# Performance work log

Hardware: AMD Instinct MI355X
Metric: run time of the kernel (lower is better)

Reference implementation:

```python
import jax, jax.numpy as jnp
import numpy as np

EPS = 1e-12

def _l2norm(x):
    # F.normalize(p=2, dim=1)
    n = jnp.sqrt(jnp.sum(x * x, axis=1, keepdims=True))
    return x / jnp.maximum(n, EPS)

def _sage(h, c, W, b):
    # Bundler: Linear(concat(h, mean_neigh)) -> l2 normalize -> relu
    z = jnp.concatenate([h, c], axis=1) @ W + b
    return jax.nn.relu(_l2norm(z))

def _block_diag(blocks):
    # blocks: [B, K, K] -> dense [B*K, B*K] block-diagonal (torch.block_diag of per-graph S^T A S)
    B, K, _ = blocks.shape
    out = jnp.zeros((B * K, B * K), blocks.dtype)
    base = (jnp.arange(B) * K)[:, None, None]
    r = base + jnp.arange(K)[None, :, None]
    c = base + jnp.arange(K)[None, None, :]
    return out.at[r, c].set(blocks)

def setup_inputs() -> dict:
    key = jax.random.key(0)
    k0, k1, k2, k3, k4 = jax.random.split(key, 5)
    B, n, F, K, E = 64, 1024, 128, 128, 16384
    N = B * n
    h = jax.random.normal(k0, (N, F), dtype=jnp.float32)
    src_local = jax.random.randint(k1, (B, E), 0, n, dtype=jnp.int32)
    dst_local = jax.random.randint(k2, (B, E), 0, n, dtype=jnp.int32)
    s = 1.0 / np.sqrt(2 * F)
    W_feat = jax.random.normal(k3, (2 * F, F), dtype=jnp.float32) * s
    b_feat = jnp.zeros((F,), dtype=jnp.float32)
    W_pool = jax.random.normal(k4, (2 * F, K), dtype=jnp.float32) * s
    b_pool = jnp.zeros((K,), dtype=jnp.float32)
    return {"h": h, "src_local": src_local, "dst_local": dst_local,
            "W_feat": W_feat, "b_feat": b_feat, "W_pool": W_pool, "b_pool": b_pool}

def reference(h, src_local, dst_local, W_feat, b_feat, W_pool, b_pool):
    N, F = h.shape
    B, E = src_local.shape
    n = N // B
    K = W_pool.shape[1]
    # per-graph local edge ids -> global ids (batched graph)
    off = (jnp.arange(B, dtype=src_local.dtype) * n)[:, None]
    src = (src_local + off).reshape(-1)  # [B*E]
    dst = (dst_local + off).reshape(-1)
    # MeanAggregator: c[i] = mean over in-neighbors (edges src->dst) of h[src]
    deg = jax.ops.segment_sum(jnp.ones((B * E,), h.dtype), dst, num_segments=N)
    c = jax.ops.segment_sum(h[src], dst, num_segments=N) / jnp.maximum(deg, 1.0)[:, None]
    feat = _sage(h, c, W_feat, b_feat)                     # [N, F]
    assign = jax.nn.softmax(_sage(h, c, W_pool, b_pool), axis=1)  # [N, K] per-graph soft assignment
    # adj_external(transpose=True): adj[u, v] = 1 for edge (u -> v)
    # AS[u] = sum over edges (u->v) of assign[v]
    AS = jax.ops.segment_sum(assign[dst], src, num_segments=N)    # [N, K]
    S_r = assign.reshape(B, n, K)
    AS_r = AS.reshape(B, n, K)
    feat_r = feat.reshape(B, n, F)
    # h_new = S^T feat (block-diagonal S => per-graph contraction)
    h_new = jnp.einsum('bnk,bnf->bkf', S_r, feat_r).reshape(B * K, F)
    # adj_new = S^T (adj S), block diagonal across graphs
    blocks = jnp.einsum('bnk,bnl->bkl', S_r, AS_r)
    adj_new = _block_diag(blocks)
    return adj_new, h_new
```

## Files before the change

kernel.cpp:

```cpp
#include <hip/hip_runtime.h>
#include <hip/hip_bf16.h>
#include <cstddef>

#define B_    64
#define NPG   1024
#define F_    128
#define K_    128
#define E_    16384
#define N_    (B_*NPG)
#define BE_   (B_*E_)
#define ADJ_DIM 8192
#define ADJ_ELEMS 67108864UL

typedef __bf16 bf16x8 __attribute__((ext_vector_type(8)));
typedef float  f32x4  __attribute__((ext_vector_type(4)));
typedef unsigned short u16x8 __attribute__((ext_vector_type(8)));

__device__ inline unsigned short f2b(float f) {
  __bf16 b = (__bf16)f;
  return *reinterpret_cast<unsigned short*>(&b);
}
__device__ inline unsigned packbf(float x, float y) {
  return (unsigned)f2b(x) | ((unsigned)f2b(y) << 16);
}
__device__ inline void addrow(float* a, uint4 v) {
  a[0] += __uint_as_float(v.x << 16);
  a[1] += __uint_as_float(v.x & 0xffff0000u);
  a[2] += __uint_as_float(v.y << 16);
  a[3] += __uint_as_float(v.y & 0xffff0000u);
  a[4] += __uint_as_float(v.z << 16);
  a[5] += __uint_as_float(v.z & 0xffff0000u);
  a[6] += __uint_as_float(v.w << 16);
  a[7] += __uint_as_float(v.w & 0xffff0000u);
}

__global__ void k_hbf(const float* __restrict__ h, unsigned short* __restrict__ hb) {
  int i = blockIdx.x * 256 + threadIdx.x;
  float4 v = reinterpret_cast<const float4*>(h)[i];
  ushort4 o;
  o.x = f2b(v.x); o.y = f2b(v.y); o.z = f2b(v.z); o.w = f2b(v.w);
  reinterpret_cast<ushort4*>(hb)[i] = o;
}

__global__ void k_count(const int* __restrict__ srcl, const int* __restrict__ dstl,
                        int* __restrict__ deg_in, int* __restrict__ deg_out) {
  int i = blockIdx.x * 256 + threadIdx.x;
  int b = i >> 14;
  int base = b << 10;
  atomicAdd(&deg_in[dstl[i] + base], 1);
  atomicAdd(&deg_out[srcl[i] + base], 1);
}

__global__ __launch_bounds__(1024) void k_scan(const int* __restrict__ deg,
                                               int* __restrict__ off, int* __restrict__ cur) {
  int b = blockIdx.x, t = threadIdx.x;
  int v = deg[b * NPG + t];
  int lane = t & 63, wid = t >> 6;
  int x = v;
  #pragma unroll
  for (int d = 1; d < 64; d <<= 1) {
    int y = __shfl_up(x, d, 64);
    if (lane >= d) x += y;
  }
  __shared__ int wsum[16];
  if (lane == 63) wsum[wid] = x;
  __syncthreads();
  if (t < 16) {
    int s = wsum[t];
    #pragma unroll
    for (int d = 1; d < 16; d <<= 1) {
      int y = __shfl_up(s, d, 16);
      if (t >= d) s += y;
    }
    wsum[t] = s;
  }
  __syncthreads();
  int woff = wid ? wsum[wid - 1] : 0;
  int o = b * E_ + woff + x - v;
  off[b * NPG + t] = o;
  cur[b * NPG + t] = o;
}

__global__ void k_build(const int* __restrict__ srcl, const int* __restrict__ dstl,
                        int* __restrict__ cur_in, int* __restrict__ cur_out,
                        int* __restrict__ ebd_src, int* __restrict__ ebs_dst) {
  int i = blockIdx.x * 256 + threadIdx.x;
  int b = i >> 14;
  int base = b << 10;
  int s = srcl[i] + base, d = dstl[i] + base;
  int p = atomicAdd(&cur_in[d], 1);
  ebd_src[p] = s;
  int q = atomicAdd(&cur_out[s], 1);
  ebs_dst[q] = d;
}

template<int ROWSTRIDE, bool MEAN, bool ZERO>
__global__ void k_gather(const unsigned short* __restrict__ rows, const int* __restrict__ elist,
                         const int* __restrict__ off, const int* __restrict__ deg,
                         unsigned short* __restrict__ outb, float* __restrict__ adj) {
  if (ZERO) {
    float4 z4 = make_float4(0.f, 0.f, 0.f, 0.f);
    float4* dst = reinterpret_cast<float4*>(adj) + (size_t)blockIdx.x * 1024 + threadIdx.x;
    #pragma unroll
    for (int r = 0; r < 4; ++r) dst[r * 256] = z4;
  }
  int w = threadIdx.x >> 6, lane = threadIdx.x & 63;
  int g = lane >> 4, li = lane & 15;
  int node = blockIdx.x * 4 + w;
  int o = off[node], d = deg[node];
  float acc[8];
  #pragma unroll
  for (int i = 0; i < 8; ++i) acc[i] = 0.f;
  const unsigned short* rbase = rows + li * 8;
  int e = o, end = o + d;
  while (e < end) {
    int cnt = end - e; if (cnt > 64) cnt = 64;
    int sidx = (lane < cnt) ? elist[e + lane] : 0;
    for (int t = 0; t * 4 < cnt; ++t) {
      int j = t * 4 + g;
      int s = __shfl(sidx, j, 64);
      if (j < cnt) {
        uint4 v = *reinterpret_cast<const uint4*>(rbase + (size_t)s * ROWSTRIDE);
        addrow(acc, v);
      }
    }
    e += cnt;
  }
  #pragma unroll
  for (int i = 0; i < 8; ++i) {
    acc[i] += __shfl_xor(acc[i], 16, 64);
    acc[i] += __shfl_xor(acc[i], 32, 64);
  }
  if (g == 0) {
    float sc = MEAN ? (1.0f / fmaxf((float)d, 1.0f)) : 1.0f;
    uint4 ov;
    ov.x = packbf(acc[0] * sc, acc[1] * sc);
    ov.y = packbf(acc[2] * sc, acc[3] * sc);
    ov.z = packbf(acc[4] * sc, acc[5] * sc);
    ov.w = packbf(acc[6] * sc, acc[7] * sc);
    *reinterpret_cast<uint4*>(outb + (size_t)node * 128 + li * 8) = ov;
  }
}

__global__ void k_wt(const float* __restrict__ Wf, const float* __restrict__ Wp,
                     __bf16* __restrict__ Wt) {
  int j = blockIdx.x;
  int k = threadIdx.x;
  const float* W = (j < 128) ? Wf : Wp;
  int jj = j & 127;
  Wt[j * 256 + k] = (__bf16)W[k * 128 + jj];
}

__global__ __launch_bounds__(512) void k_gemm(const __bf16* __restrict__ hb,
                                              const __bf16* __restrict__ cb,
                                              const __bf16* __restrict__ Wt,
                                              const float* __restrict__ bfeat,
                                              const float* __restrict__ bpool,
                                              __bf16* __restrict__ Z) {
  __shared__ char smem[69632];
  __bf16* A_lds = (__bf16*)smem;
  __bf16* B_lds = (__bf16*)(smem + 8192);
  const int t = threadIdx.x;
  const int wid = t >> 6, lane = t & 63;
  const int wm = wid >> 1, wn = wid & 1;
  const int lo = lane & 15, hi = lane >> 4;
  const int m0 = blockIdx.x * 128;

  float bias[8];
  const float* bsrc = wn ? bpool : bfeat;
  #pragma unroll
  for (int nf = 0; nf < 8; ++nf) bias[nf] = bsrc[nf * 16 + lo];

  f32x4 acc[2][8];
  #pragma unroll
  for (int mf = 0; mf < 2; ++mf)
    #pragma unroll
    for (int nf = 0; nf < 8; ++nf) acc[mf][nf] = (f32x4){0.f, 0.f, 0.f, 0.f};

  const int am = t >> 2, akq = (t & 3) * 8;
  const int bj = t >> 1, bh = (t & 1) * 16;

  for (int ks = 0; ks < 8; ++ks) {
    const int kb = ks * 32;
    const __bf16* __restrict__ X = (kb < 128) ? hb : cb;
    const int kbb = kb & 127;
    *reinterpret_cast<bf16x8*>(A_lds + am * 32 + akq) =
        *reinterpret_cast<const bf16x8*>(X + (size_t)(m0 + am) * 128 + kbb + akq);
    {
      bf16x8 b0 = *reinterpret_cast<const bf16x8*>(Wt + bj * 256 + kb + bh);
      bf16x8 b1 = *reinterpret_cast<const bf16x8*>(Wt + bj * 256 + kb + bh + 8);
      *reinterpret_cast<bf16x8*>(B_lds + bj * 40 + bh) = b0;
      *reinterpret_cast<bf16x8*>(B_lds + bj * 40 + bh + 8) = b1;
    }
    __syncthreads();
    bf16x8 a[2], b[8];
    #pragma unroll
    for (int mf = 0; mf < 2; ++mf)
      a[mf] = *reinterpret_cast<const bf16x8*>(A_lds + (wm * 32 + mf * 16 + lo) * 32 + hi * 8);
    #pragma unroll
    for (int nf = 0; nf < 8; ++nf)
      b[nf] = *reinterpret_cast<const bf16x8*>(B_lds + (wn * 128 + nf * 16 + lo) * 40 + hi * 8);
    #pragma unroll
    for (int mf = 0; mf < 2; ++mf)
      #pragma unroll
      for (int nf = 0; nf < 8; ++nf)
        acc[mf][nf] = __builtin_amdgcn_mfma_f32_16x16x32_bf16(a[mf], b[nf], acc[mf][nf], 0, 0, 0);
    __syncthreads();
  }

  __bf16* obuf = (__bf16*)(smem + wid * 8704);
  #pragma unroll
  for (int mf = 0; mf < 2; ++mf) {
    #pragma unroll
    for (int r = 0; r < 4; ++r) {
      float v[8];
      #pragma unroll
      for (int nf = 0; nf < 8; ++nf) v[nf] = acc[mf][nf][r] + bias[nf];
      float ss = 0.f;
      #pragma unroll
      for (int nf = 0; nf < 8; ++nf) ss += v[nf] * v[nf];
      ss += __shfl_xor(ss, 1, 64); ss += __shfl_xor(ss, 2, 64);
      ss += __shfl_xor(ss, 4, 64); ss += __shfl_xor(ss, 8, 64);
      float rn = 1.0f / fmaxf(sqrtf(ss), 1e-12f);
      #pragma unroll
      for (int nf = 0; nf < 8; ++nf) v[nf] = fmaxf(v[nf] * rn, 0.f);
      if (wn) {
        float mx = v[0];
        #pragma unroll
        for (int nf = 1; nf < 8; ++nf) mx = fmaxf(mx, v[nf]);
        mx = fmaxf(mx, __shfl_xor(mx, 1, 64)); mx = fmaxf(mx, __shfl_xor(mx, 2, 64));
        mx = fmaxf(mx, __shfl_xor(mx, 4, 64)); mx = fmaxf(mx, __shfl_xor(mx, 8, 64));
        float es = 0.f;
        #pragma unroll
        for (int nf = 0; nf < 8; ++nf) { v[nf] = __expf(v[nf] - mx); es += v[nf]; }
        es += __shfl_xor(es, 1, 64); es += __shfl_xor(es, 2, 64);
        es += __shfl_xor(es, 4, 64); es += __shfl_xor(es, 8, 64);
        float inv = 1.0f / es;
        #pragma unroll
        for (int nf = 0; nf < 8; ++nf) v[nf] *= inv;
      }
      int row = mf * 16 + hi * 4 + r;
      #pragma unroll
      for (int nf = 0; nf < 8; ++nf) obuf[row * 136 + nf * 16 + lo] = (__bf16)v[nf];
    }
  }
  __syncthreads();
  #pragma unroll
  for (int i = 0; i < 8; ++i) {
    int r = i * 4 + hi;
    bf16x8 d = *reinterpret_cast<const bf16x8*>(obuf + r * 136 + lo * 8);
    int node = m0 + wm * 32 + r;
    *reinterpret_cast<bf16x8*>(Z + (size_t)node * 256 + wn * 128 + lo * 8) = d;
  }
}

__global__ __launch_bounds__(256) void k_poolm(const unsigned short* __restrict__ Zb,
                                               const unsigned short* __restrict__ ASb,
                                               float* __restrict__ h_new,
                                               float* __restrict__ adj) {
  const int blk = blockIdx.x;
  const int b = blk >> 2, ch = (blk >> 1) & 1, nh = blk & 1;
  const int n0 = b * NPG + nh * 512;
  __shared__ __align__(16) unsigned short ST[128 * 40];
  __shared__ __align__(16) unsigned short XT[128 * 40];
  const int t = threadIdx.x;
  const int wid = t >> 6, lane = t & 63;
  const int lo = lane & 15, hi = lane >> 4;
  const int wk = wid >> 1, wf = wid & 1;
  const int sn = t & 31, sc0 = (t >> 5) * 16;

  f32x4 acc[4][4];
  #pragma unroll
  for (int m = 0; m < 4; ++m)
    #pragma unroll
    for (int f = 0; f < 4; ++f) acc[m][f] = (f32x4){0.f, 0.f, 0.f, 0.f};

  for (int nc = 0; nc < 512; nc += 32) {
    int n = n0 + nc + sn;
    {
      u16x8 s0 = *reinterpret_cast<const u16x8*>(Zb + (size_t)n * 256 + 128 + sc0);
      u16x8 s1 = *reinterpret_cast<const u16x8*>(Zb + (size_t)n * 256 + 128 + sc0 + 8);
      #pragma unroll
      for (int i = 0; i < 8; ++i) ST[(sc0 + i) * 40 + sn] = s0[i];
      #pragma unroll
      for (int i = 0; i < 8; ++i) ST[(sc0 + 8 + i) * 40 + sn] = s1[i];
    }
    {
      const unsigned short* xr = ch ? (ASb + (size_t)n * 128 + sc0)
                                    : (Zb + (size_t)n * 256 + sc0);
      u16x8 x0 = *reinterpret_cast<const u16x8*>(xr);
      u16x8 x1 = *reinterpret_cast<const u16x8*>(xr + 8);
      #pragma unroll
      for (int i = 0; i < 8; ++i) XT[(sc0 + i) * 40 + sn] = x0[i];
      #pragma unroll
      for (int i = 0; i < 8; ++i) XT[(sc0 + 8 + i) * 40 + sn] = x1[i];
    }
    __syncthreads();
    bf16x8 a[4], bb[4];
    #pragma unroll
    for (int m = 0; m < 4; ++m)
      a[m] = *reinterpret_cast<const bf16x8*>(ST + (wk * 64 + m * 16 + lo) * 40 + hi * 8);
    #pragma unroll
    for (int f = 0; f < 4; ++f)
      bb[f] = *reinterpret_cast<const bf16x8*>(XT + (wf * 64 + f * 16 + lo) * 40 + hi * 8);
    #pragma unroll
    for (int m = 0; m < 4; ++m)
      #pragma unroll
      for (int f = 0; f < 4; ++f)
        acc[m][f] = __builtin_amdgcn_mfma_f32_16x16x32_bf16(a[m], bb[f], acc[m][f], 0, 0, 0);
    __syncthreads();
  }

  if (ch == 0) {
    #pragma unroll
    for (int m = 0; m < 4; ++m)
      #pragma unroll
      for (int f = 0; f < 4; ++f)
        #pragma unroll
        for (int r = 0; r < 4; ++r) {
          int k = wk * 64 + m * 16 + hi * 4 + r;
          int fc = wf * 64 + f * 16 + lo;
          atomicAdd(&h_new[(size_t)(b * 128 + k) * 128 + fc], acc[m][f][r]);
        }
  } else {
    #pragma unroll
    for (int m = 0; m < 4; ++m)
      #pragma unroll
      for (int f = 0; f < 4; ++f)
        #pragma unroll
        for (int r = 0; r < 4; ++r) {
          int k = wk * 64 + m * 16 + hi * 4 + r;
          int fc = wf * 64 + f * 16 + lo;
          atomicAdd(&adj[(size_t)(b * 128 + k) * ADJ_DIM + b * 128 + fc], acc[m][f][r]);
        }
  }
}

extern "C" void kernel_launch(void* const* d_in, const int* in_sizes, int n_in,
                              void* d_out, int out_size, void* d_ws, size_t ws_size,
                              hipStream_t stream) {
  (void)in_sizes; (void)n_in; (void)out_size; (void)ws_size;
  const float* h   = (const float*)d_in[0];
  const int* srcl  = (const int*)d_in[1];
  const int* dstl  = (const int*)d_in[2];
  const float* Wf  = (const float*)d_in[3];
  const float* bfe = (const float*)d_in[4];
  const float* Wp  = (const float*)d_in[5];
  const float* bpo = (const float*)d_in[6];

  float* out   = (float*)d_out;
  float* adj   = out;
  float* h_new = out + ADJ_ELEMS;

  char* W = (char*)d_ws;
  int* deg_in   = (int*)W;
  int* deg_out  = deg_in + N_;
  int* off_in   = deg_out + N_;
  int* cur_in   = off_in + N_;
  int* off_out  = cur_in + N_;
  int* cur_out  = off_out + N_;
  int* ebd_src  = cur_out + N_;
  int* ebs_dst  = ebd_src + BE_;
  unsigned short* hb  = (unsigned short*)(ebs_dst + BE_);
  unsigned short* cb  = hb + 8388608UL;
  unsigned short* Zb  = cb + 8388608UL;
  unsigned short* ASb = Zb + 16777216UL;
  __bf16* Wt          = (__bf16*)(ASb + 8388608UL);

  hipMemsetAsync(deg_in, 0, 2UL * N_ * sizeof(int), stream);
  hipMemsetAsync(h_new, 0, (size_t)B_ * K_ * F_ * sizeof(float), stream);
  k_hbf<<<8192, 256, 0, stream>>>(h, hb);
  k_wt<<<256, 256, 0, stream>>>(Wf, Wp, Wt);
  k_count<<<BE_ / 256, 256, 0, stream>>>(srcl, dstl, deg_in, deg_out);
  k_scan<<<B_, 1024, 0, stream>>>(deg_in, off_in, cur_in);
  k_scan<<<B_, 1024, 0, stream>>>(deg_out, off_out, cur_out);
  k_build<<<BE_ / 256, 256, 0, stream>>>(srcl, dstl, cur_in, cur_out, ebd_src, ebs_dst);
  k_gather<128, true, true><<<N_ / 4, 256, 0, stream>>>(hb, ebd_src, off_in, deg_in, cb, adj);
  k_gemm<<<N_ / 128, 512, 0, stream>>>((const __bf16*)hb, (const __bf16*)cb, Wt, bfe, bpo, (__bf16*)Zb);
  k_gather<256, false, false><<<N_ / 4, 256, 0, stream>>>(Zb + 128, ebs_dst, off_out, deg_out, ASb, nullptr);
  k_poolm<<<256, 256, 0, stream>>>(Zb, ASb, h_new, adj);
}
```

Before: 570.1 us.

## Replace CSR edge gathers with dense per-graph adjacency GEMMs on MFMA

Drops the CSR pipeline (degree counts, scans, bucket build, two sparse row gathers). Instead it scatters edge counts into a dense 1024x1024 fp32 adjacency block per graph and computes the neighbour mean and the A·S term as bf16 MFMA GEMMs. The h-to-bf16 conversion is folded into the feature GEMM's A-tile load, and zeroing of the adj output moves into that GEMM. This trades irregular gathers and atomics for a 256 MB dense matrix that must be zeroed and then read twice, so memory traffic goes up.

```diff
diff --git a/kernel.cpp b/kernel.cpp
--- a/kernel.cpp
+++ b/kernel.cpp
@@ -20,127 +20,6 @@
   __bf16 b = (__bf16)f;
   return *reinterpret_cast<unsigned short*>(&b);
 }
-__device__ inline unsigned packbf(float x, float y) {
-  return (unsigned)f2b(x) | ((unsigned)f2b(y) << 16);
-}
-__device__ inline void addrow(float* a, uint4 v) {
-  a[0] += __uint_as_float(v.x << 16);
-  a[1] += __uint_as_float(v.x & 0xffff0000u);
-  a[2] += __uint_as_float(v.y << 16);
-  a[3] += __uint_as_float(v.y & 0xffff0000u);
-  a[4] += __uint_as_float(v.z << 16);
-  a[5] += __uint_as_float(v.z & 0xffff0000u);
-  a[6] += __uint_as_float(v.w << 16);
-  a[7] += __uint_as_float(v.w & 0xffff0000u);
-}
-
-__global__ void k_hbf(const float* __restrict__ h, unsigned short* __restrict__ hb) {
-  int i = blockIdx.x * 256 + threadIdx.x;
-  float4 v = reinterpret_cast<const float4*>(h)[i];
-  ushort4 o;
-  o.x = f2b(v.x); o.y = f2b(v.y); o.z = f2b(v.z); o.w = f2b(v.w);
-  reinterpret_cast<ushort4*>(hb)[i] = o;
-}
-
-__global__ void k_count(const int* __restrict__ srcl, const int* __restrict__ dstl,
-                        int* __restrict__ deg_in, int* __restrict__ deg_out) {
-  int i = blockIdx.x * 256 + threadIdx.x;
-  int b = i >> 14;
-  int base = b << 10;
-  atomicAdd(&deg_in[dstl[i] + base], 1);
-  atomicAdd(&deg_out[srcl[i] + base], 1);
-}
-
-__global__ __launch_bounds__(1024) void k_scan(const int* __restrict__ deg,
-                                               int* __restrict__ off, int* __restrict__ cur) {
-  int b = blockIdx.x, t = threadIdx.x;
-  int v = deg[b * NPG + t];
-  int lane = t & 63, wid = t >> 6;
-  int x = v;
-  #pragma unroll
-  for (int d = 1; d < 64; d <<= 1) {
-    int y = __shfl_up(x, d, 64);
-    if (lane >= d) x += y;
-  }
-  __shared__ int wsum[16];
-  if (lane == 63) wsum[wid] = x;
-  __syncthreads();
-  if (t < 16) {
-    int s = wsum[t];
-    #pragma unroll
-    for (int d = 1; d < 16; d <<= 1) {
-      int y = __shfl_up(s, d, 16);
-      if (t >= d) s += y;
-    }
-    wsum[t] = s;
-  }
-  __syncthreads();
-  int woff = wid ? wsum[wid - 1] : 0;
-  int o = b * E_ + woff + x - v;
-  off[b * NPG + t] = o;
-  cur[b * NPG + t] = o;
-}
-
-__global__ void k_build(const int* __restrict__ srcl, const int* __restrict__ dstl,
-                        int* __restrict__ cur_in, int* __restrict__ cur_out,
-                        int* __restrict__ ebd_src, int* __restrict__ ebs_dst) {
-  int i = blockIdx.x * 256 + threadIdx.x;
-  int b = i >> 14;
-  int base = b << 10;
-  int s = srcl[i] + base, d = dstl[i] + base;
-  int p = atomicAdd(&cur_in[d], 1);
-  ebd_src[p] = s;
-  int q = atomicAdd(&cur_out[s], 1);
-  ebs_dst[q] = d;
-}
-
-template<int ROWSTRIDE, bool MEAN, bool ZERO>
-__global__ void k_gather(const unsigned short* __restrict__ rows, const int* __restrict__ elist,
-                         const int* __restrict__ off, const int* __restrict__ deg,
-                         unsigned short* __restrict__ outb, float* __restrict__ adj) {
-  if (ZERO) {
-    float4 z4 = make_float4(0.f, 0.f, 0.f, 0.f);
-    float4* dst = reinterpret_cast<float4*>(adj) + (size_t)blockIdx.x * 1024 + threadIdx.x;
-    #pragma unroll
-    for (int r = 0; r < 4; ++r) dst[r * 256] = z4;
-  }
-  int w = threadIdx.x >> 6, lane = threadIdx.x & 63;
-  int g = lane >> 4, li = lane & 15;
-  int node = blockIdx.x * 4 + w;
-  int o = off[node], d = deg[node];
-  float acc[8];
-  #pragma unroll
-  for (int i = 0; i < 8; ++i) acc[i] = 0.f;
-  const unsigned short* rbase = rows + li * 8;
-  int e = o, end = o + d;
-  while (e < end) {
-    int cnt = end - e; if (cnt > 64) cnt = 64;
-    int sidx = (lane < cnt) ? elist[e + lane] : 0;
-    for (int t = 0; t * 4 < cnt; ++t) {
-      int j = t * 4 + g;
-      int s = __shfl(sidx, j, 64);
-      if (j < cnt) {
-        uint4 v = *reinterpret_cast<const uint4*>(rbase + (size_t)s * ROWSTRIDE);
-        addrow(acc, v);
-      }
-    }
-    e += cnt;
-  }
-  #pragma unroll
-  for (int i = 0; i < 8; ++i) {
-    acc[i] += __shfl_xor(acc[i], 16, 64);
-    acc[i] += __shfl_xor(acc[i], 32, 64);
-  }
-  if (g == 0) {
-    float sc = MEAN ? (1.0f / fmaxf((float)d, 1.0f)) : 1.0f;
-    uint4 ov;
-    ov.x = packbf(acc[0] * sc, acc[1] * sc);
-    ov.y = packbf(acc[2] * sc, acc[3] * sc);
-    ov.z = packbf(acc[4] * sc, acc[5] * sc);
-    ov.w = packbf(acc[6] * sc, acc[7] * sc);
-    *reinterpret_cast<uint4*>(outb + (size_t)node * 128 + li * 8) = ov;
-  }
-}
 
 __global__ void k_wt(const float* __restrict__ Wf, const float* __restrict__ Wp,
                      __bf16* __restrict__ Wt) {
@@ -151,12 +30,117 @@
   Wt[j * 256 + k] = (__bf16)W[k * 128 + jj];
 }
 
-__global__ __launch_bounds__(512) void k_gemm(const __bf16* __restrict__ hb,
-                                              const __bf16* __restrict__ cb,
+__global__ void k_count(const int* __restrict__ dstl, int* __restrict__ deg_in,
+                        float* __restrict__ M) {
+  int i = blockIdx.x * 256 + threadIdx.x;
+  float4 z4 = make_float4(0.f, 0.f, 0.f, 0.f);
+  float4* mz = reinterpret_cast<float4*>(M) + (size_t)blockIdx.x * 4096 + threadIdx.x;
+  #pragma unroll
+  for (int r = 0; r < 16; ++r) mz[r * 256] = z4;
+  int b = i >> 14;
+  atomicAdd(&deg_in[(b << 10) + dstl[i]], 1);
+}
+
+__global__ void k_scatterM(const int* __restrict__ srcl, const int* __restrict__ dstl,
+                           float* __restrict__ M) {
+  int i = blockIdx.x * 256 + threadIdx.x;
+  int b = i >> 14;
+  atomicAdd(&M[(size_t)b * (NPG * (size_t)NPG) + (size_t)dstl[i] * NPG + srcl[i]], 1.0f);
+}
+
+__global__ __launch_bounds__(256) void k_cgemm(const float* __restrict__ M,
+                                               const float* __restrict__ h,
+                                               const int* __restrict__ deg,
+                                               unsigned short* __restrict__ cb) {
+  const int blk = blockIdx.x;
+  const int g = blk >> 3, mt = blk & 7;
+  const float* __restrict__ Mg = M + (size_t)g * NPG * NPG + (size_t)mt * 128 * NPG;
+  const float* __restrict__ hg = h + (size_t)g * NPG * 128;
+  __shared__ __align__(16) unsigned short Am[128 * 40];
+  __shared__ __align__(16) unsigned short Bt[128 * 40];
+  const int t = threadIdx.x;
+  const int wid = t >> 6, lane = t & 63;
+  const int lo = lane & 15, hi = lane >> 4;
+  const int wk = wid >> 1, wf = wid & 1;
+  const int ar = t >> 1, ac = (t & 1) * 16;
+  const int sn = t & 31, sc0 = (t >> 5) * 16;
+
+  f32x4 acc[4][4];
+  #pragma unroll
+  for (int m = 0; m < 4; ++m)
+    #pragma unroll
+    for (int f = 0; f < 4; ++f) acc[m][f] = (f32x4){0.f, 0.f, 0.f, 0.f};
+
+  for (int s0 = 0; s0 < NPG; s0 += 32) {
+    {
+      const float* arow = Mg + (size_t)ar * NPG + s0 + ac;
+      float4 v0 = *reinterpret_cast<const float4*>(arow);
+      float4 v1 = *reinterpret_cast<const float4*>(arow + 4);
+      float4 v2 = *reinterpret_cast<const float4*>(arow + 8);
+      float4 v3 = *reinterpret_cast<const float4*>(arow + 12);
+      u16x8 p0, p1;
+      p0[0] = f2b(v0.x); p0[1] = f2b(v0.y); p0[2] = f2b(v0.z); p0[3] = f2b(v0.w);
+      p0[4] = f2b(v1.x); p0[5] = f2b(v1.y); p0[6] = f2b(v1.z); p0[7] = f2b(v1.w);
+      p1[0] = f2b(v2.x); p1[1] = f2b(v2.y); p1[2] = f2b(v2.z); p1[3] = f2b(v2.w);
+      p1[4] = f2b(v3.x); p1[5] = f2b(v3.y); p1[6] = f2b(v3.z); p1[7] = f2b(v3.w);
+      *reinterpret_cast<u16x8*>(Am + ar * 40 + ac) = p0;
+      *reinterpret_cast<u16x8*>(Am + ar * 40 + ac + 8) = p1;
+    }
+    {
+      const float* brow = hg + (size_t)(s0 + sn) * 128 + sc0;
+      float4 w0 = *reinterpret_cast<const float4*>(brow);
+      float4 w1 = *reinterpret_cast<const float4*>(brow + 4);
+      float4 w2 = *reinterpret_cast<const float4*>(brow + 8);
+      float4 w3 = *reinterpret_cast<const float4*>(brow + 12);
+      float e[16] = {w0.x, w0.y, w0.z, w0.w, w1.x, w1.y, w1.z, w1.w,
+                     w2.x, w2.y, w2.z, w2.w, w3.x, w3.y, w3.z, w3.w};
+      #pragma unroll
+      for (int i2 = 0; i2 < 16; ++i2) Bt[(sc0 + i2) * 40 + sn] = f2b(e[i2]);
+    }
+    __syncthreads();
+    bf16x8 a[4], bb[4];
+    #pragma unroll
+    for (int m = 0; m < 4; ++m)
+      a[m] = *reinterpret_cast<const bf16x8*>(Am + (wk * 64 + m * 16 + lo) * 40 + hi * 8);
+    #pragma unroll
+    for (int f = 0; f < 4; ++f)
+      bb[f] = *reinterpret_cast<const bf16x8*>(Bt + (wf * 64 + f * 16 + lo) * 40 + hi * 8);
+    #pragma unroll
+    for (int m = 0; m < 4; ++m)
+      #pragma unroll
+      for (int f = 0; f < 4; ++f)
+        acc[m][f] = __builtin_amdgcn_mfma_f32_16x16x32_bf16(a[m], bb[f], acc[m][f], 0, 0, 0);
+    __syncthreads();
+  }
+
+  #pragma unroll
+  for (int m = 0; m < 4; ++m)
+    #pragma unroll
+    for (int r = 0; r < 4; ++r) {
+      int mrow = wk * 64 + m * 16 + hi * 4 + r;
+      int node = g * NPG + mt * 128 + mrow;
+      float inv = 1.0f / fmaxf((float)deg[node], 1.0f);
+      #pragma unroll
+      for (int f = 0; f < 4; ++f) {
+        int fc = wf * 64 + f * 16 + lo;
+        cb[(size_t)node * 128 + fc] = f2b(acc[m][f][r] * inv);
+      }
+    }
+}
+
+__global__ __launch_bounds__(512) void k_gemm(const float* __restrict__ h,
+                                              const unsigned short* __restrict__ cb,
                                               const __bf16* __restrict__ Wt,
                                               const float* __restrict__ bfeat,
                                               const float* __restrict__ bpool,
-                                              __bf16* __restrict__ Z) {
+                                              __bf16* __restrict__ Z,
+                                              float* __restrict__ adj) {
+  {
+    float4 z4 = make_float4(0.f, 0.f, 0.f, 0.f);
+    float4* dst = reinterpret_cast<float4*>(adj) + (size_t)blockIdx.x * 32768 + threadIdx.x;
+    #pragma unroll 8
+    for (int r = 0; r < 64; ++r) dst[r * 512] = z4;
+  }
   __shared__ char smem[69632];
   __bf16* A_lds = (__bf16*)smem;
   __bf16* B_lds = (__bf16*)(smem + 8192);
@@ -182,10 +166,18 @@
 
   for (int ks = 0; ks < 8; ++ks) {
     const int kb = ks * 32;
-    const __bf16* __restrict__ X = (kb < 128) ? hb : cb;
-    const int kbb = kb & 127;
-    *reinterpret_cast<bf16x8*>(A_lds + am * 32 + akq) =
-        *reinterpret_cast<const bf16x8*>(X + (size_t)(m0 + am) * 128 + kbb + akq);
+    if (kb < 128) {
+      const float* arow = h + (size_t)(m0 + am) * 128 + kb + akq;
+      float4 v0 = *reinterpret_cast<const float4*>(arow);
+      float4 v1 = *reinterpret_cast<const float4*>(arow + 4);
+      bf16x8 bv;
+      bv[0] = (__bf16)v0.x; bv[1] = (__bf16)v0.y; bv[2] = (__bf16)v0.z; bv[3] = (__bf16)v0.w;
+      bv[4] = (__bf16)v1.x; bv[5] = (__bf16)v1.y; bv[6] = (__bf16)v1.z; bv[7] = (__bf16)v1.w;
+      *reinterpret_cast<bf16x8*>(A_lds + am * 32 + akq) = bv;
+    } else {
+      *reinterpret_cast<bf16x8*>(A_lds + am * 32 + akq) =
+          *reinterpret_cast<const bf16x8*>((const __bf16*)cb + (size_t)(m0 + am) * 128 + (kb - 128) + akq);
+    }
     {
       bf16x8 b0 = *reinterpret_cast<const bf16x8*>(Wt + bj * 256 + kb + bh);
       bf16x8 b1 = *reinterpret_cast<const bf16x8*>(Wt + bj * 256 + kb + bh + 8);
@@ -254,6 +246,76 @@
   }
 }
 
+__global__ __launch_bounds__(256) void k_asgemm(const float* __restrict__ M,
+                                                const unsigned short* __restrict__ Zb,
+                                                unsigned short* __restrict__ ASb) {
+  const int blk = blockIdx.x;
+  const int g = blk >> 3, ut = blk & 7;
+  const float* __restrict__ Mg = M + (size_t)g * NPG * NPG;
+  const unsigned short* __restrict__ Sg = Zb + (size_t)g * NPG * 256 + 128;
+  __shared__ __align__(16) unsigned short AT[128 * 40];
+  __shared__ __align__(16) unsigned short ST[128 * 40];
+  const int t = threadIdx.x;
+  const int wid = t >> 6, lane = t & 63;
+  const int lo = lane & 15, hi = lane >> 4;
+  const int wk = wid >> 1, wf = wid & 1;
+  const int sn = t & 31, sc0 = (t >> 5) * 16;
+
+  f32x4 acc[4][4];
+  #pragma unroll
+  for (int m = 0; m < 4; ++m)
+    #pragma unroll
+    for (int f = 0; f < 4; ++f) acc[m][f] = (f32x4){0.f, 0.f, 0.f, 0.f};
+
+  for (int v0 = 0; v0 < NPG; v0 += 32) {
+    {
+      const float* arow = Mg + (size_t)(v0 + sn) * NPG + ut * 128 + sc0;
+      float4 a0 = *reinterpret_cast<const float4*>(arow);
+      float4 a1 = *reinterpret_cast<const float4*>(arow + 4);
+      float4 a2 = *reinterpret_cast<const float4*>(arow + 8);
+      float4 a3 = *reinterpret_cast<const float4*>(arow + 12);
+      float e[16] = {a0.x, a0.y, a0.z, a0.w, a1.x, a1.y, a1.z, a1.w,
+                     a2.x, a2.y, a2.z, a2.w, a3.x, a3.y, a3.z, a3.w};
+      #pragma unroll
+      for (int i2 = 0; i2 < 16; ++i2) AT[(sc0 + i2) * 40 + sn] = f2b(e[i2]);
+    }
+    {
+      const unsigned short* srow = Sg + (size_t)(v0 + sn) * 256 + sc0;
+      u16x8 s0v = *reinterpret_cast<const u16x8*>(srow);
+      u16x8 s1v = *reinterpret_cast<const u16x8*>(srow + 8);
+      #pragma unroll
+      for (int i2 = 0; i2 < 8; ++i2) ST[(sc0 + i2) * 40 + sn] = s0v[i2];
+      #pragma unroll
+      for (int i2 = 0; i2 < 8; ++i2) ST[(sc0 + 8 + i2) * 40 + sn] = s1v[i2];
+    }
+    __syncthreads();
+    bf16x8 a[4], bb[4];
+    #pragma unroll
+    for (int m = 0; m < 4; ++m)
+      a[m] = *reinterpret_cast<const bf16x8*>(AT + (wk * 64 + m * 16 + lo) * 40 + hi * 8);
+    #pragma unroll
+    for (int f = 0; f < 4; ++f)
+      bb[f] = *reinterpret_cast<const bf16x8*>(ST + (wf * 64 + f * 16 + lo) * 40 + hi * 8);
+    #pragma unroll
+    for (int m = 0; m < 4; ++m)
+      #pragma unroll
+      for (int f = 0; f < 4; ++f)
+        acc[m][f] = __builtin_amdgcn_mfma_f32_16x16x32_bf16(a[m], bb[f], acc[m][f], 0, 0, 0);
+    __syncthreads();
+  }
+
+  #pragma unroll
+  for (int m = 0; m < 4; ++m)
+    #pragma unroll
+    for (int f = 0; f < 4; ++f)
+      #pragma unroll
+      for (int r = 0; r < 4; ++r) {
+        int u = ut * 128 + wk * 64 + m * 16 + hi * 4 + r;
+        int kc = wf * 64 + f * 16 + lo;
+        ASb[(size_t)(g * NPG + u) * 128 + kc] = f2b(acc[m][f][r]);
+      }
+}
+
 __global__ __launch_bounds__(256) void k_poolm(const unsigned short* __restrict__ Zb,
                                                const unsigned short* __restrict__ ASb,
                                                float* __restrict__ h_new,
@@ -352,31 +414,21 @@
   float* adj   = out;
   float* h_new = out + ADJ_ELEMS;
 
-  char* W = (char*)d_ws;
-  int* deg_in   = (int*)W;
-  int* deg_out  = deg_in + N_;
-  int* off_in   = deg_out + N_;
-  int* cur_in   = off_in + N_;
-  int* off_out  = cur_in + N_;
-  int* cur_out  = off_out + N_;
-  int* ebd_src  = cur_out + N_;
-  int* ebs_dst  = ebd_src + BE_;
-  unsigned short* hb  = (unsigned short*)(ebs_dst + BE_);
-  unsigned short* cb  = hb + 8388608UL;
+  char* Wp8 = (char*)d_ws;
+  int* deg_in         = (int*)Wp8;
+  float* M            = (float*)(Wp8 + (1UL << 20));
+  unsigned short* cb  = (unsigned short*)(Wp8 + (1UL << 20) + 268435456UL);
   unsigned short* Zb  = cb + 8388608UL;
   unsigned short* ASb = Zb + 16777216UL;
   __bf16* Wt          = (__bf16*)(ASb + 8388608UL);
 
-  hipMemsetAsync(deg_in, 0, 2UL * N_ * sizeof(int), stream);
+  hipMemsetAsync(deg_in, 0, (size_t)N_ * sizeof(int), stream);
   hipMemsetAsync(h_new, 0, (size_t)B_ * K_ * F_ * sizeof(float), stream);
-  k_hbf<<<8192, 256, 0, stream>>>(h, hb);
   k_wt<<<256, 256, 0, stream>>>(Wf, Wp, Wt);
-  k_count<<<BE_ / 256, 256, 0, stream>>>(srcl, dstl, deg_in, deg_out);
-  k_scan<<<B_, 1024, 0, stream>>>(deg_in, off_in, cur_in);
-  k_scan<<<B_, 1024, 0, stream>>>(deg_out, off_out, cur_out);
-  k_build<<<BE_ / 256, 256, 0, stream>>>(srcl, dstl, cur_in, cur_out, ebd_src, ebs_dst);
-  k_gather<128, true, true><<<N_ / 4, 256, 0, stream>>>(hb, ebd_src, off_in, deg_in, cb, adj);
-  k_gemm<<<N_ / 128, 512, 0, stream>>>((const __bf16*)hb, (const __bf16*)cb, Wt, bfe, bpo, (__bf16*)Zb);
-  k_gather<256, false, false><<<N_ / 4, 256, 0, stream>>>(Zb + 128, ebs_dst, off_out, deg_out, ASb, nullptr);
+  k_count<<<BE_ / 256, 256, 0, stream>>>(dstl, deg_in, M);
+  k_scatterM<<<BE_ / 256, 256, 0, stream>>>(srcl, dstl, M);
+  k_cgemm<<<512, 256, 0, stream>>>(M, h, deg_in, cb);
+  k_gemm<<<512, 512, 0, stream>>>(h, cb, Wt, bfe, bpo, (__bf16*)Zb, adj);
+  k_asgemm<<<512, 256, 0, stream>>>(M, Zb, ASb);
   k_poolm<<<256, 256, 0, stream>>>(Zb, ASb, h_new, adj);
 }
```

Result: slower. 667.9 us (+17.2%).

## Fuse preprocessing kernels, spread adj zeroing across kernels, drop pooling atomics

Applied to the files above, without the earlier changes.

Merges the bf16 conversion of h, the weight transpose, degree counting and part of the adj zeroing into one k_pre launch. It also merges the two scans into one launch and spreads the rest of the 256MB adj zero-fill across k_build and k_gemm. The pooling kernel now has each block cover a whole graph with 512 threads and write results directly, so the h_new memset and the atomics go away. Launch count falls and the zero-fill can overlap compute, at the cost of only 128 blocks in the pooling stage and much more work packed into k_gemm.

```diff
diff --git a/kernel.cpp b/kernel.cpp
--- a/kernel.cpp
+++ b/kernel.cpp
@@ -34,27 +34,54 @@
   a[7] += __uint_as_float(v.w & 0xffff0000u);
 }
 
-__global__ void k_hbf(const float* __restrict__ h, unsigned short* __restrict__ hb) {
-  int i = blockIdx.x * 256 + threadIdx.x;
-  float4 v = reinterpret_cast<const float4*>(h)[i];
-  ushort4 o;
-  o.x = f2b(v.x); o.y = f2b(v.y); o.z = f2b(v.z); o.w = f2b(v.w);
-  reinterpret_cast<ushort4*>(hb)[i] = o;
-}
-
-__global__ void k_count(const int* __restrict__ srcl, const int* __restrict__ dstl,
-                        int* __restrict__ deg_in, int* __restrict__ deg_out) {
-  int i = blockIdx.x * 256 + threadIdx.x;
-  int b = i >> 14;
-  int base = b << 10;
-  atomicAdd(&deg_in[dstl[i] + base], 1);
-  atomicAdd(&deg_out[srcl[i] + base], 1);
-}
-
-__global__ __launch_bounds__(1024) void k_scan(const int* __restrict__ deg,
-                                               int* __restrict__ off, int* __restrict__ cur) {
-  int b = blockIdx.x, t = threadIdx.x;
-  int v = deg[b * NPG + t];
+__global__ void k_pre(const float* __restrict__ h, const float* __restrict__ Wf,
+                      const float* __restrict__ Wp, const int* __restrict__ srcl,
+                      const int* __restrict__ dstl, unsigned short* __restrict__ hb,
+                      __bf16* __restrict__ Wt, int* __restrict__ deg_in,
+                      int* __restrict__ deg_out, float* __restrict__ adj) {
+  const int bid = blockIdx.x, tid = threadIdx.x;
+  if (bid < 2048) {
+    #pragma unroll
+    for (int r = 0; r < 4; ++r) {
+      int i = bid * 1024 + r * 256 + tid;
+      float4 v = reinterpret_cast<const float4*>(h)[i];
+      ushort4 o;
+      o.x = f2b(v.x); o.y = f2b(v.y); o.z = f2b(v.z); o.w = f2b(v.w);
+      reinterpret_cast<ushort4*>(hb)[i] = o;
+    }
+  } else if (bid < 2304) {
+    int j = bid - 2048;
+    const float* W = (j < 128) ? Wf : Wp;
+    int jj = j & 127;
+    Wt[j * 256 + tid] = (__bf16)W[tid * 128 + jj];
+  } else if (bid < 2560) {
+    int e0 = (bid - 2304) * 4096 + tid;
+    #pragma unroll
+    for (int r = 0; r < 16; ++r) {
+      int i = e0 + r * 256;
+      int b = i >> 14;
+      int base = b << 10;
+      atomicAdd(&deg_in[dstl[i] + base], 1);
+      atomicAdd(&deg_out[srcl[i] + base], 1);
+    }
+  } else {
+    float4 z4 = make_float4(0.f, 0.f, 0.f, 0.f);
+    float4* a4 = reinterpret_cast<float4*>(adj);
+    size_t base = (size_t)(bid - 2560) * 4096 + tid;
+    #pragma unroll
+    for (int r = 0; r < 16; ++r) a4[base + r * 256] = z4;
+  }
+}
+
+__global__ __launch_bounds__(1024) void k_scan2(const int* __restrict__ deg_in,
+                                                const int* __restrict__ deg_out,
+                                                int* __restrict__ off_in, int* __restrict__ cur_in,
+                                                int* __restrict__ off_out, int* __restrict__ cur_out) {
+  int dir = blockIdx.x >> 6, g = blockIdx.x & 63, t = threadIdx.x;
+  const int* deg = dir ? deg_out : deg_in;
+  int* off = dir ? off_out : off_in;
+  int* cur = dir ? cur_out : cur_in;
+  int v = deg[g * NPG + t];
   int lane = t & 63, wid = t >> 6;
   int x = v;
   #pragma unroll
@@ -76,34 +103,40 @@
   }
   __syncthreads();
   int woff = wid ? wsum[wid - 1] : 0;
-  int o = b * E_ + woff + x - v;
-  off[b * NPG + t] = o;
-  cur[b * NPG + t] = o;
+  int o = g * E_ + woff + x - v;
+  off[g * NPG + t] = o;
+  cur[g * NPG + t] = o;
 }
 
 __global__ void k_build(const int* __restrict__ srcl, const int* __restrict__ dstl,
                         int* __restrict__ cur_in, int* __restrict__ cur_out,
-                        int* __restrict__ ebd_src, int* __restrict__ ebs_dst) {
-  int i = blockIdx.x * 256 + threadIdx.x;
-  int b = i >> 14;
-  int base = b << 10;
-  int s = srcl[i] + base, d = dstl[i] + base;
-  int p = atomicAdd(&cur_in[d], 1);
-  ebd_src[p] = s;
-  int q = atomicAdd(&cur_out[s], 1);
-  ebs_dst[q] = d;
-}
-
-template<int ROWSTRIDE, bool MEAN, bool ZERO>
+                        int* __restrict__ ebd_src, int* __restrict__ ebs_dst,
+                        float* __restrict__ adj) {
+  const int bid = blockIdx.x, tid = threadIdx.x;
+  {
+    float4 z4 = make_float4(0.f, 0.f, 0.f, 0.f);
+    float4* a4 = reinterpret_cast<float4*>(adj);
+    size_t base = 6291456UL + (size_t)bid * 2048 + tid;
+    #pragma unroll
+    for (int r = 0; r < 8; ++r) a4[base + r * 256] = z4;
+  }
+  #pragma unroll
+  for (int r = 0; r < 2; ++r) {
+    int i = bid * 512 + r * 256 + tid;
+    int b = i >> 14;
+    int base = b << 10;
+    int s = srcl[i] + base, d = dstl[i] + base;
+    int p = atomicAdd(&cur_in[d], 1);
+    ebd_src[p] = s;
+    int q = atomicAdd(&cur_out[s], 1);
+    ebs_dst[q] = d;
+  }
+}
+
+template<int ROWSTRIDE, bool MEAN>
 __global__ void k_gather(const unsigned short* __restrict__ rows, const int* __restrict__ elist,
                          const int* __restrict__ off, const int* __restrict__ deg,
-                         unsigned short* __restrict__ outb, float* __restrict__ adj) {
-  if (ZERO) {
-    float4 z4 = make_float4(0.f, 0.f, 0.f, 0.f);
-    float4* dst = reinterpret_cast<float4*>(adj) + (size_t)blockIdx.x * 1024 + threadIdx.x;
-    #pragma unroll
-    for (int r = 0; r < 4; ++r) dst[r * 256] = z4;
-  }
+                         unsigned short* __restrict__ outb) {
   int w = threadIdx.x >> 6, lane = threadIdx.x & 63;
   int g = lane >> 4, li = lane & 15;
   int node = blockIdx.x * 4 + w;
@@ -142,21 +175,20 @@
   }
 }
 
-__global__ void k_wt(const float* __restrict__ Wf, const float* __restrict__ Wp,
-                     __bf16* __restrict__ Wt) {
-  int j = blockIdx.x;
-  int k = threadIdx.x;
-  const float* W = (j < 128) ? Wf : Wp;
-  int jj = j & 127;
-  Wt[j * 256 + k] = (__bf16)W[k * 128 + jj];
-}
-
 __global__ __launch_bounds__(512) void k_gemm(const __bf16* __restrict__ hb,
                                               const __bf16* __restrict__ cb,
                                               const __bf16* __restrict__ Wt,
                                               const float* __restrict__ bfeat,
                                               const float* __restrict__ bpool,
-                                              __bf16* __restrict__ Z) {
+                                              __bf16* __restrict__ Z,
+                                              float* __restrict__ adj) {
+  {
+    float4 z4 = make_float4(0.f, 0.f, 0.f, 0.f);
+    float4* a4 = reinterpret_cast<float4*>(adj);
+    size_t base = 10485760UL + (size_t)blockIdx.x * 12288 + threadIdx.x;
+    #pragma unroll 8
+    for (int r = 0; r < 24; ++r) a4[base + r * 512] = z4;
+  }
   __shared__ char smem[69632];
   __bf16* A_lds = (__bf16*)smem;
   __bf16* B_lds = (__bf16*)(smem + 8192);
@@ -254,86 +286,70 @@
   }
 }
 
-__global__ __launch_bounds__(256) void k_poolm(const unsigned short* __restrict__ Zb,
+__global__ __launch_bounds__(512) void k_poolm(const unsigned short* __restrict__ Zb,
                                                const unsigned short* __restrict__ ASb,
                                                float* __restrict__ h_new,
                                                float* __restrict__ adj) {
   const int blk = blockIdx.x;
-  const int b = blk >> 2, ch = (blk >> 1) & 1, nh = blk & 1;
-  const int n0 = b * NPG + nh * 512;
+  const int b = blk >> 1, ch = blk & 1;
+  const int n0 = b * NPG;
   __shared__ __align__(16) unsigned short ST[128 * 40];
   __shared__ __align__(16) unsigned short XT[128 * 40];
   const int t = threadIdx.x;
   const int wid = t >> 6, lane = t & 63;
   const int lo = lane & 15, hi = lane >> 4;
-  const int wk = wid >> 1, wf = wid & 1;
-  const int sn = t & 31, sc0 = (t >> 5) * 16;
-
-  f32x4 acc[4][4];
+  const int wk = wid >> 2, wf = wid & 3;
+  const int sn = t & 31, sc0 = (t >> 5) * 8;
+
+  f32x4 acc[4][2];
   #pragma unroll
   for (int m = 0; m < 4; ++m)
     #pragma unroll
-    for (int f = 0; f < 4; ++f) acc[m][f] = (f32x4){0.f, 0.f, 0.f, 0.f};
-
-  for (int nc = 0; nc < 512; nc += 32) {
+    for (int f = 0; f < 2; ++f) acc[m][f] = (f32x4){0.f, 0.f, 0.f, 0.f};
+
+  for (int nc = 0; nc < NPG; nc += 32) {
     int n = n0 + nc + sn;
     {
       u16x8 s0 = *reinterpret_cast<const u16x8*>(Zb + (size_t)n * 256 + 128 + sc0);
-      u16x8 s1 = *reinterpret_cast<const u16x8*>(Zb + (size_t)n * 256 + 128 + sc0 + 8);
       #pragma unroll
       for (int i = 0; i < 8; ++i) ST[(sc0 + i) * 40 + sn] = s0[i];
-      #pragma unroll
-      for (int i = 0; i < 8; ++i) ST[(sc0 + 8 + i) * 40 + sn] = s1[i];
     }
     {
       const unsigned short* xr = ch ? (ASb + (size_t)n * 128 + sc0)
                                     : (Zb + (size_t)n * 256 + sc0);
       u16x8 x0 = *reinterpret_cast<const u16x8*>(xr);
-      u16x8 x1 = *reinterpret_cast<const u16x8*>(xr + 8);
       #pragma unroll
       for (int i = 0; i < 8; ++i) XT[(sc0 + i) * 40 + sn] = x0[i];
-      #pragma unroll
-      for (int i = 0; i < 8; ++i) XT[(sc0 + 8 + i) * 40 + sn] = x1[i];
     }
     __syncthreads();
-    bf16x8 a[4], bb[4];
+    bf16x8 a[4], bb[2];
     #pragma unroll
     for (int m = 0; m < 4; ++m)
       a[m] = *reinterpret_cast<const bf16x8*>(ST + (wk * 64 + m * 16 + lo) * 40 + hi * 8);
     #pragma unroll
-    for (int f = 0; f < 4; ++f)
-      bb[f] = *reinterpret_cast<const bf16x8*>(XT + (wf * 64 + f * 16 + lo) * 40 + hi * 8);
+    for (int f = 0; f < 2; ++f)
+      bb[f] = *reinterpret_cast<const bf16x8*>(XT + (wf * 32 + f * 16 + lo) * 40 + hi * 8);
     #pragma unroll
     for (int m = 0; m < 4; ++m)
       #pragma unroll
-      for (int f = 0; f < 4; ++f)
+      for (int f = 0; f < 2; ++f)
         acc[m][f] = __builtin_amdgcn_mfma_f32_16x16x32_bf16(a[m], bb[f], acc[m][f], 0, 0, 0);
     __syncthreads();
   }
 
-  if (ch == 0) {
-    #pragma unroll
-    for (int m = 0; m < 4; ++m)
-      #pragma unroll
-      for (int f = 0; f < 4; ++f)
-        #pragma unroll
-        for (int r = 0; r < 4; ++r) {
-          int k = wk * 64 + m * 16 + hi * 4 + r;
-          int fc = wf * 64 + f * 16 + lo;
-          atomicAdd(&h_new[(size_t)(b * 128 + k) * 128 + fc], acc[m][f][r]);
-        }
-  } else {
-    #pragma unroll
-    for (int m = 0; m < 4; ++m)
-      #pragma unroll
-      for (int f = 0; f < 4; ++f)
-        #pragma unroll
-        for (int r = 0; r < 4; ++r) {
-          int k = wk * 64 + m * 16 + hi * 4 + r;
-          int fc = wf * 64 + f * 16 + lo;
-          atomicAdd(&adj[(size_t)(b * 128 + k) * ADJ_DIM + b * 128 + fc], acc[m][f][r]);
-        }
-  }
+  #pragma unroll
+  for (int m = 0; m < 4; ++m)
+    #pragma unroll
+    for (int f = 0; f < 2; ++f)
+      #pragma unroll
+      for (int r = 0; r < 4; ++r) {
+        int k = wk * 64 + m * 16 + hi * 4 + r;
+        int fc = wf * 32 + f * 16 + lo;
+        if (ch == 0)
+          h_new[(size_t)(b * 128 + k) * 128 + fc] = acc[m][f][r];
+        else
+          adj[(size_t)(b * 128 + k) * ADJ_DIM + b * 128 + fc] = acc[m][f][r];
+      }
 }
 
 extern "C" void kernel_launch(void* const* d_in, const int* in_sizes, int n_in,
@@ -368,15 +384,11 @@
   __bf16* Wt          = (__bf16*)(ASb + 8388608UL);
 
   hipMemsetAsync(deg_in, 0, 2UL * N_ * sizeof(int), stream);
-  hipMemsetAsync(h_new, 0, (size_t)B_ * K_ * F_ * sizeof(float), stream);
-  k_hbf<<<8192, 256, 0, stream>>>(h, hb);
-  k_wt<<<256, 256, 0, stream>>>(Wf, Wp, Wt);
-  k_count<<<BE_ / 256, 256, 0, stream>>>(srcl, dstl, deg_in, deg_out);
-  k_scan<<<B_, 1024, 0, stream>>>(deg_in, off_in, cur_in);
-  k_scan<<<B_, 1024, 0, stream>>>(deg_out, off_out, cur_out);
-  k_build<<<BE_ / 256, 256, 0, stream>>>(srcl, dstl, cur_in, cur_out, ebd_src, ebs_dst);
-  k_gather<128, true, true><<<N_ / 4, 256, 0, stream>>>(hb, ebd_src, off_in, deg_in, cb, adj);
-  k_gemm<<<N_ / 128, 512, 0, stream>>>((const __bf16*)hb, (const __bf16*)cb, Wt, bfe, bpo, (__bf16*)Zb);
-  k_gather<256, false, false><<<N_ / 4, 256, 0, stream>>>(Zb + 128, ebs_dst, off_out, deg_out, ASb, nullptr);
-  k_poolm<<<256, 256, 0, stream>>>(Zb, ASb, h_new, adj);
-}
+  k_pre<<<4096, 256, 0, stream>>>(h, Wf, Wp, srcl, dstl, hb, Wt, deg_in, deg_out, adj);
+  k_scan2<<<128, 1024, 0, stream>>>(deg_in, deg_out, off_in, cur_in, off_out, cur_out);
+  k_build<<<2048, 256, 0, stream>>>(srcl, dstl, cur_in, cur_out, ebd_src, ebs_dst, adj);
+  k_gather<128, true><<<N_ / 4, 256, 0, stream>>>(hb, ebd_src, off_in, deg_in, cb);
+  k_gemm<<<512, 512, 0, stream>>>((const __bf16*)hb, (const __bf16*)cb, Wt, bfe, bpo, (__bf16*)Zb, adj);
+  k_gather<256, false><<<N_ / 4, 256, 0, stream>>>(Zb + 128, ebs_dst, off_out, deg_out, ASb);
+  k_poolm<<<128, 512, 0, stream>>>(Zb, ASb, h_new, adj);
+}
```

Result: faster. 545.2 us (-4.4%).
